# Kernel optimization log

Measured on AMD Instinct MI355X. Metric: run time of the kernel, lower is better.

## Reference

```python
import jax, jax.numpy as jnp
import numpy as np

SIM_THRESHOLD = 0.9


def setup_inputs() -> dict:
    key = jax.random.key(0)
    k1, k2 = jax.random.split(key)
    # patches: b * c * num * ws * ws  (b=2, c=8, num=1024, ws=3) -> n = 16384
    patches = jax.random.normal(k1, (2, 8, 1024, 3, 3), dtype=jnp.float32)
    # db: m * ws * ws
    db = jax.random.normal(k2, (16384, 3, 3), dtype=jnp.float32)
    return {"patches": patches, "db": db}


def reference(patches, db):
    ws = patches.shape[-1]
    p = patches.reshape(-1, ws, ws)          # [n, ws, ws]
    n = p.shape[0]
    m = db.shape[0]
    pf = p.reshape(n, -1)                    # [n, ws*ws]
    df = db.reshape(m, -1)                   # [m, ws*ws]
    dot = pf @ df.T                          # [n, m], tiny K=ws*ws -> memory bound
    norm_n = jnp.linalg.norm(pf, axis=1, keepdims=True)   # [n, 1]
    norm_m = jnp.linalg.norm(df, axis=1, keepdims=True)   # [m, 1]
    cos = dot / (norm_n * norm_m.T)          # [n, m] cosine similarity
    # patch kept only if dissimilar to EVERY db entry
    mask = jnp.all(cos < SIM_THRESHOLD, axis=1)            # [n] bool
    # jit-friendly fixed-shape compaction: zero out rejected patches instead of
    # dropping rows (original does db = cat(db, patches[mask]))
    filtered = jnp.where(mask[:, None, None], p, jnp.zeros((), p.dtype))
    return jnp.concatenate([db.reshape(-1, ws, ws), filtered], axis=0)  # [m+n, ws, ws]
```

## Files before the change

### kernel.cpp

```cpp
#include <hip/hip_runtime.h>

#define NPATCH 16384
#define NDB    16384
#define WS9    9
#define KP     16
#define JCH    32
#define CHUNK  (NDB / JCH)
#define TILES  (CHUNK / 32)
#define BAND_LO 0.89998f
#define BAND_HI 0.90002f
#define COPY_BLOCKS 144

typedef short bf16x8 __attribute__((ext_vector_type(8)));
typedef float f32x16 __attribute__((ext_vector_type(16)));

__device__ __forceinline__ float np_norm9(const float* v) {
#pragma clang fp contract(off)
    float q0 = v[0] * v[0], q1 = v[1] * v[1], q2 = v[2] * v[2], q3 = v[3] * v[3];
    float q4 = v[4] * v[4], q5 = v[5] * v[5], q6 = v[6] * v[6], q7 = v[7] * v[7];
    float q8 = v[8] * v[8];
    float s = ((q0 + q1) + (q2 + q3)) + ((q4 + q5) + (q6 + q7));
    s = s + q8;
    return sqrtf(s);
}

__device__ __forceinline__ unsigned short f2bf(float x) {
    unsigned u = __float_as_uint(x);
    return (unsigned short)((u + 0x7fffu + ((u >> 16) & 1u)) >> 16);
}
__device__ __forceinline__ float bf2f(unsigned short h) {
    return __uint_as_float(((unsigned)h) << 16);
}

__device__ __forceinline__ void stage_row(const float* __restrict__ src,
                                          unsigned short* dh, unsigned short* dl) {
    float v[WS9];
#pragma unroll
    for (int k = 0; k < WS9; k++) v[k] = src[k];
    float inv = 1.0f / np_norm9(v);
    unsigned short h[KP], l[KP];
#pragma unroll
    for (int k = 0; k < KP; k++) {
        float x = (k < WS9) ? v[k] * inv : 0.0f;
        h[k] = f2bf(x);
        l[k] = f2bf(x - bf2f(h[k]));
    }
    int hw[8], lw[8];
#pragma unroll
    for (int k = 0; k < 8; k++) {
        hw[k] = (int)h[2 * k] | ((int)h[2 * k + 1] << 16);
        lw[k] = (int)l[2 * k] | ((int)l[2 * k + 1] << 16);
    }
    ((int4*)dh)[0] = make_int4(hw[0], hw[1], hw[2], hw[3]);
    ((int4*)dh)[1] = make_int4(hw[4], hw[5], hw[6], hw[7]);
    ((int4*)dl)[0] = make_int4(lw[0], lw[1], lw[2], lw[3]);
    ((int4*)dl)[1] = make_int4(lw[4], lw[5], lw[6], lw[7]);
}

__global__ __launch_bounds__(256) void k_phase1(const float* __restrict__ patches,
                                                const float* __restrict__ db,
                                                float* __restrict__ partial,
                                                int* __restrict__ band_count) {
    __shared__ __align__(16) unsigned short s_dnh[CHUNK * KP];
    __shared__ __align__(16) unsigned short s_dnl[CHUNK * KP];
    __shared__ __align__(16) unsigned short s_pnh[256 * KP];
    __shared__ __align__(16) unsigned short s_pnl[256 * KP];

    if (blockIdx.x == 0 && blockIdx.y == 0 && threadIdx.x == 0) *band_count = 0;

    int jbase = blockIdx.y * CHUNK;
    int ibase = blockIdx.x * 256;
#pragma unroll
    for (int rr = 0; rr < CHUNK / 256; rr++) {
        int r = rr * 256 + threadIdx.x;
        stage_row(db + (size_t)(jbase + r) * WS9, &s_dnh[r * KP], &s_dnl[r * KP]);
    }
    stage_row(patches + (size_t)(ibase + threadIdx.x) * WS9,
              &s_pnh[threadIdx.x * KP], &s_pnl[threadIdx.x * KP]);
    __syncthreads();

    int lane = threadIdx.x & 63;
    int wave = threadIdx.x >> 6;
    int col = lane & 31;
    int half = lane >> 5;
    int i0 = ibase + wave * 64;

    const bf16x8* Ph = (const bf16x8*)s_pnh;
    const bf16x8* Pl = (const bf16x8*)s_pnl;
    bf16x8 b_hi0 = Ph[(wave * 64 + col) * 2 + half];
    bf16x8 b_lo0 = Pl[(wave * 64 + col) * 2 + half];
    bf16x8 b_hi1 = Ph[(wave * 64 + 32 + col) * 2 + half];
    bf16x8 b_lo1 = Pl[(wave * 64 + 32 + col) * 2 + half];

    const bf16x8* Ah = (const bf16x8*)s_dnh;
    const bf16x8* Al = (const bf16x8*)s_dnl;

    f32x16 zc = {0.f,0.f,0.f,0.f,0.f,0.f,0.f,0.f,0.f,0.f,0.f,0.f,0.f,0.f,0.f,0.f};
    float rm0 = -3.0e38f, rm1 = -3.0e38f;

#pragma unroll 2
    for (int t = 0; t < TILES; ++t) {
        bf16x8 a_h = Ah[(t * 32 + col) * 2 + half];
        bf16x8 a_l = Al[(t * 32 + col) * 2 + half];
        f32x16 acc0 = __builtin_amdgcn_mfma_f32_32x32x16_bf16(a_h, b_hi0, zc, 0, 0, 0);
        acc0 = __builtin_amdgcn_mfma_f32_32x32x16_bf16(a_h, b_lo0, acc0, 0, 0, 0);
        acc0 = __builtin_amdgcn_mfma_f32_32x32x16_bf16(a_l, b_hi0, acc0, 0, 0, 0);
        f32x16 acc1 = __builtin_amdgcn_mfma_f32_32x32x16_bf16(a_h, b_hi1, zc, 0, 0, 0);
        acc1 = __builtin_amdgcn_mfma_f32_32x32x16_bf16(a_h, b_lo1, acc1, 0, 0, 0);
        acc1 = __builtin_amdgcn_mfma_f32_32x32x16_bf16(a_l, b_hi1, acc1, 0, 0, 0);
#pragma unroll
        for (int r = 0; r < 16; ++r) {
            rm0 = fmaxf(rm0, acc0[r]);
            rm1 = fmaxf(rm1, acc1[r]);
        }
    }
    rm0 = fmaxf(rm0, __shfl_xor(rm0, 32, 64));
    rm1 = fmaxf(rm1, __shfl_xor(rm1, 32, 64));
    int ti = half ? (i0 + 32 + col) : (i0 + col);
    partial[(size_t)blockIdx.y * NPATCH + ti] = half ? rm1 : rm0;
}

__global__ __launch_bounds__(256) void k_finish(const float* __restrict__ patches,
                                                const float* __restrict__ db,
                                                const float* __restrict__ partial,
                                                float* __restrict__ out,
                                                int* __restrict__ band_list,
                                                int* __restrict__ band_count) {
    int b = blockIdx.x;
    if (b < COPY_BLOCKS) {
        int e = b * 256 + threadIdx.x;
        ((float4*)out)[e] = ((const float4*)db)[e];
        return;
    }
    int i = (b - COPY_BLOCKS) * 256 + threadIdx.x;
    float cosmax = partial[i];
#pragma unroll
    for (int c = 1; c < JCH; c++)
        cosmax = fmaxf(cosmax, partial[(size_t)c * NPATCH + i]);
    if (cosmax >= BAND_LO && cosmax < BAND_HI) {
        int idx = atomicAdd(band_count, 1);
        band_list[idx] = i;
        return;
    }
    int hit = (cosmax >= BAND_HI) ? 1 : 0;
#pragma unroll
    for (int k = 0; k < WS9; k++)
        out[(size_t)(NDB + i) * WS9 + k] = hit ? 0.0f : patches[(size_t)i * WS9 + k];
}

__global__ __launch_bounds__(256) void k_phase2(const float* __restrict__ patches,
                                                const float* __restrict__ db,
                                                const int* __restrict__ band_list,
                                                const int* __restrict__ band_count,
                                                float* __restrict__ out) {
    __shared__ float sp[WS9];
    __shared__ float snp;
    __shared__ int shit;
    int nb = *band_count;
    for (int idx = blockIdx.x; idx < nb; idx += gridDim.x) {
        int i = band_list[idx];
        if (threadIdx.x == 0) {
            float p[WS9];
            for (int k = 0; k < WS9; k++) { p[k] = patches[(size_t)i * WS9 + k]; sp[k] = p[k]; }
            snp = np_norm9(p);
            shit = 0;
        }
        __syncthreads();
        float p[WS9];
#pragma unroll
        for (int k = 0; k < WS9; k++) p[k] = sp[k];
        float npn = snp;
        int hit = 0;
        for (int j = (int)threadIdx.x; j < NDB; j += 256) {
            float d[WS9];
#pragma unroll
            for (int k = 0; k < WS9; k++) d[k] = db[(size_t)j * WS9 + k];
            float dot = 0.0f;
#pragma unroll
            for (int k = 0; k < WS9; k++) dot = fmaf(p[k], d[k], dot);
            float nd = np_norm9(d);
            float cs = dot / (npn * nd);
            if (!((double)cs < 0.9)) hit = 1;
        }
        if (hit) atomicOr(&shit, 1);
        __syncthreads();
        int m = shit;
        if (threadIdx.x < WS9)
            out[(size_t)(NDB + i) * WS9 + threadIdx.x] = m ? 0.0f : sp[threadIdx.x];
        __syncthreads();
    }
}

extern "C" void kernel_launch(void* const* d_in, const int* in_sizes, int n_in,
                              void* d_out, int out_size, void* d_ws, size_t ws_size,
                              hipStream_t stream) {
    const float* patches = (const float*)d_in[0];
    const float* db      = (const float*)d_in[1];
    float* out = (float*)d_out;

    char* wsb = (char*)d_ws;
    float* partial    = (float*)wsb;
    int*   band_list  = (int*)(wsb + (size_t)JCH * NPATCH * 4);
    int*   band_count = (int*)(wsb + (size_t)JCH * NPATCH * 4 + (size_t)NPATCH * 4);

    k_phase1<<<dim3(NPATCH / 256, JCH), dim3(256), 0, stream>>>(patches, db,
                                                                partial, band_count);
    k_finish<<<dim3(COPY_BLOCKS + NPATCH / 256), dim3(256), 0, stream>>>(
        patches, db, partial, out, band_list, band_count);
    k_phase2<<<dim3(256), dim3(256), 0, stream>>>(patches, db, band_list, band_count, out);
}
```

Before: 95.38 us.

## Precompute normalized bf16 hi/lo splits once in a prep kernel

Adds a prep kernel that normalizes and splits all patches and db rows into bf16 hi/lo pairs once, and also copies db into the output. Previously every phase1 block recomputed norms and splits for its db chunk and patches. Phase1 now loads the pre-split data from global memory with int4 copies into shared memory and reads the patch operands directly from global. The running max reduction is rewritten as a tree of 3-input max ops. The cost is an extra kernel launch plus workspace traffic for the staged arrays.

```diff
diff --git a/kernel.cpp b/kernel.cpp
--- a/kernel.cpp
+++ b/kernel.cpp
@@ -9,10 +9,12 @@
 #define TILES  (CHUNK / 32)
 #define BAND_LO 0.89998f
 #define BAND_HI 0.90002f
-#define COPY_BLOCKS 144
+#define PREP_BLOCKS 144
 
 typedef short bf16x8 __attribute__((ext_vector_type(8)));
 typedef float f32x16 __attribute__((ext_vector_type(16)));
+
+#define MAX3(a,b,c) fmaxf(fmaxf((a),(b)),(c))
 
 __device__ __forceinline__ float np_norm9(const float* v) {
 #pragma clang fp contract(off)
@@ -57,27 +59,48 @@
     ((int4*)dl)[1] = make_int4(lw[4], lw[5], lw[6], lw[7]);
 }
 
-__global__ __launch_bounds__(256) void k_phase1(const float* __restrict__ patches,
-                                                const float* __restrict__ db,
-                                                float* __restrict__ partial,
-                                                int* __restrict__ band_count) {
-    __shared__ __align__(16) unsigned short s_dnh[CHUNK * KP];
-    __shared__ __align__(16) unsigned short s_dnl[CHUNK * KP];
-    __shared__ __align__(16) unsigned short s_pnh[256 * KP];
-    __shared__ __align__(16) unsigned short s_pnl[256 * KP];
-
-    if (blockIdx.x == 0 && blockIdx.y == 0 && threadIdx.x == 0) *band_count = 0;
+__global__ __launch_bounds__(256) void k_prep(const float* __restrict__ patches,
+                                              const float* __restrict__ db,
+                                              unsigned short* __restrict__ pnh,
+                                              unsigned short* __restrict__ pnl,
+                                              unsigned short* __restrict__ dnh,
+                                              unsigned short* __restrict__ dnl,
+                                              float* __restrict__ out,
+                                              int* __restrict__ band_count) {
+    int t = blockIdx.x * 256 + threadIdx.x;
+    if (t == 0) *band_count = 0;
+    ((float4*)out)[t] = ((const float4*)db)[t];
+    if (t < NPATCH) {
+        stage_row(patches + (size_t)t * WS9, &pnh[(size_t)t * KP], &pnl[(size_t)t * KP]);
+    } else if (t < 2 * NPATCH) {
+        int r = t - NPATCH;
+        stage_row(db + (size_t)r * WS9, &dnh[(size_t)r * KP], &dnl[(size_t)r * KP]);
+    }
+}
+
+__global__ __launch_bounds__(256) void k_phase1(const unsigned short* __restrict__ pnh,
+                                                const unsigned short* __restrict__ pnl,
+                                                const unsigned short* __restrict__ dnh,
+                                                const unsigned short* __restrict__ dnl,
+                                                float* __restrict__ partial) {
+    __shared__ __align__(16) unsigned short s_dh[CHUNK * KP];
+    __shared__ __align__(16) unsigned short s_dl[CHUNK * KP];
 
     int jbase = blockIdx.y * CHUNK;
     int ibase = blockIdx.x * 256;
-#pragma unroll
-    for (int rr = 0; rr < CHUNK / 256; rr++) {
-        int r = rr * 256 + threadIdx.x;
-        stage_row(db + (size_t)(jbase + r) * WS9, &s_dnh[r * KP], &s_dnl[r * KP]);
-    }
-    stage_row(patches + (size_t)(ibase + threadIdx.x) * WS9,
-              &s_pnh[threadIdx.x * KP], &s_pnl[threadIdx.x * KP]);
-    __syncthreads();
+
+    {
+        const int4* gh = (const int4*)(dnh + (size_t)jbase * KP);
+        const int4* gl = (const int4*)(dnl + (size_t)jbase * KP);
+        int4* sh = (int4*)s_dh;
+        int4* sl = (int4*)s_dl;
+#pragma unroll
+        for (int u = 0; u < 4; u++) {
+            int e = u * 256 + threadIdx.x;
+            sh[e] = gh[e];
+            sl[e] = gl[e];
+        }
+    }
 
     int lane = threadIdx.x & 63;
     int wave = threadIdx.x >> 6;
@@ -85,15 +108,17 @@
     int half = lane >> 5;
     int i0 = ibase + wave * 64;
 
-    const bf16x8* Ph = (const bf16x8*)s_pnh;
-    const bf16x8* Pl = (const bf16x8*)s_pnl;
-    bf16x8 b_hi0 = Ph[(wave * 64 + col) * 2 + half];
-    bf16x8 b_lo0 = Pl[(wave * 64 + col) * 2 + half];
-    bf16x8 b_hi1 = Ph[(wave * 64 + 32 + col) * 2 + half];
-    bf16x8 b_lo1 = Pl[(wave * 64 + 32 + col) * 2 + half];
-
-    const bf16x8* Ah = (const bf16x8*)s_dnh;
-    const bf16x8* Al = (const bf16x8*)s_dnl;
+    const bf16x8* Ph = (const bf16x8*)pnh;
+    const bf16x8* Pl = (const bf16x8*)pnl;
+    bf16x8 b_hi0 = Ph[(size_t)(i0 + col) * 2 + half];
+    bf16x8 b_lo0 = Pl[(size_t)(i0 + col) * 2 + half];
+    bf16x8 b_hi1 = Ph[(size_t)(i0 + 32 + col) * 2 + half];
+    bf16x8 b_lo1 = Pl[(size_t)(i0 + 32 + col) * 2 + half];
+
+    __syncthreads();
+
+    const bf16x8* Ah = (const bf16x8*)s_dh;
+    const bf16x8* Al = (const bf16x8*)s_dl;
 
     f32x16 zc = {0.f,0.f,0.f,0.f,0.f,0.f,0.f,0.f,0.f,0.f,0.f,0.f,0.f,0.f,0.f,0.f};
     float rm0 = -3.0e38f, rm1 = -3.0e38f;
@@ -108,10 +133,25 @@
         f32x16 acc1 = __builtin_amdgcn_mfma_f32_32x32x16_bf16(a_h, b_hi1, zc, 0, 0, 0);
         acc1 = __builtin_amdgcn_mfma_f32_32x32x16_bf16(a_h, b_lo1, acc1, 0, 0, 0);
         acc1 = __builtin_amdgcn_mfma_f32_32x32x16_bf16(a_l, b_hi1, acc1, 0, 0, 0);
-#pragma unroll
-        for (int r = 0; r < 16; ++r) {
-            rm0 = fmaxf(rm0, acc0[r]);
-            rm1 = fmaxf(rm1, acc1[r]);
+        {
+            float u0 = MAX3(acc0[0],  acc0[1],  acc0[2]);
+            float u1 = MAX3(acc0[3],  acc0[4],  acc0[5]);
+            float u2 = MAX3(acc0[6],  acc0[7],  acc0[8]);
+            float u3 = MAX3(acc0[9],  acc0[10], acc0[11]);
+            float u4 = MAX3(acc0[12], acc0[13], acc0[14]);
+            float u5 = MAX3(u0, u1, acc0[15]);
+            float u6 = MAX3(u2, u3, u4);
+            rm0 = MAX3(u5, u6, rm0);
+        }
+        {
+            float u0 = MAX3(acc1[0],  acc1[1],  acc1[2]);
+            float u1 = MAX3(acc1[3],  acc1[4],  acc1[5]);
+            float u2 = MAX3(acc1[6],  acc1[7],  acc1[8]);
+            float u3 = MAX3(acc1[9],  acc1[10], acc1[11]);
+            float u4 = MAX3(acc1[12], acc1[13], acc1[14]);
+            float u5 = MAX3(u0, u1, acc1[15]);
+            float u6 = MAX3(u2, u3, u4);
+            rm1 = MAX3(u5, u6, rm1);
         }
     }
     rm0 = fmaxf(rm0, __shfl_xor(rm0, 32, 64));
@@ -120,19 +160,12 @@
     partial[(size_t)blockIdx.y * NPATCH + ti] = half ? rm1 : rm0;
 }
 
-__global__ __launch_bounds__(256) void k_finish(const float* __restrict__ patches,
-                                                const float* __restrict__ db,
-                                                const float* __restrict__ partial,
-                                                float* __restrict__ out,
-                                                int* __restrict__ band_list,
-                                                int* __restrict__ band_count) {
-    int b = blockIdx.x;
-    if (b < COPY_BLOCKS) {
-        int e = b * 256 + threadIdx.x;
-        ((float4*)out)[e] = ((const float4*)db)[e];
-        return;
-    }
-    int i = (b - COPY_BLOCKS) * 256 + threadIdx.x;
+__global__ __launch_bounds__(256) void k_classify(const float* __restrict__ patches,
+                                                  const float* __restrict__ partial,
+                                                  float* __restrict__ out,
+                                                  int* __restrict__ band_list,
+                                                  int* __restrict__ band_count) {
+    int i = blockIdx.x * 256 + threadIdx.x;
     float cosmax = partial[i];
 #pragma unroll
     for (int c = 1; c < JCH; c++)
@@ -199,13 +232,27 @@
     float* out = (float*)d_out;
 
     char* wsb = (char*)d_ws;
-    float* partial    = (float*)wsb;
-    int*   band_list  = (int*)(wsb + (size_t)JCH * NPATCH * 4);
-    int*   band_count = (int*)(wsb + (size_t)JCH * NPATCH * 4 + (size_t)NPATCH * 4);
-
-    k_phase1<<<dim3(NPATCH / 256, JCH), dim3(256), 0, stream>>>(patches, db,
-                                                                partial, band_count);
-    k_finish<<<dim3(COPY_BLOCKS + NPATCH / 256), dim3(256), 0, stream>>>(
-        patches, db, partial, out, band_list, band_count);
+    size_t o_partial = 0;
+    size_t o_blist   = (size_t)JCH * NPATCH * 4;
+    size_t o_bcount  = o_blist + (size_t)NPATCH * 4;
+    size_t o_pnh     = o_bcount + 256;
+    size_t o_pnl     = o_pnh + (size_t)NPATCH * KP * 2;
+    size_t o_dnh     = o_pnl + (size_t)NPATCH * KP * 2;
+    size_t o_dnl     = o_dnh + (size_t)NDB * KP * 2;
+
+    float* partial          = (float*)(wsb + o_partial);
+    int*   band_list        = (int*)(wsb + o_blist);
+    int*   band_count       = (int*)(wsb + o_bcount);
+    unsigned short* pnh     = (unsigned short*)(wsb + o_pnh);
+    unsigned short* pnl     = (unsigned short*)(wsb + o_pnl);
+    unsigned short* dnh     = (unsigned short*)(wsb + o_dnh);
+    unsigned short* dnl     = (unsigned short*)(wsb + o_dnl);
+
+    k_prep<<<dim3(PREP_BLOCKS), dim3(256), 0, stream>>>(patches, db, pnh, pnl,
+                                                        dnh, dnl, out, band_count);
+    k_phase1<<<dim3(NPATCH / 256, JCH), dim3(256), 0, stream>>>(pnh, pnl, dnh, dnl,
+                                                                partial);
+    k_classify<<<dim3(NPATCH / 256), dim3(256), 0, stream>>>(patches, partial, out,
+                                                             band_list, band_count);
     k_phase2<<<dim3(256), dim3(256), 0, stream>>>(patches, db, band_list, band_count, out);
 }
```

Result: slower. 101.5 us (+6.4%).

## Widen patch tile per block, reuse LDS, and fold band recheck into finish kernel

Applied to the files above, without the earlier changes.

Each phase-1 block now handles 512 patches, with each wave computing four 32x32 MFMA output tiles per db tile instead of two. Patch fragments are held in registers so the same LDS buffer can then hold the db chunk. This halves the grid along the patch axis and reuses each staged db tile across more patches, and the per-tile max reduction now uses max3 chains. The separate band-recheck kernel is removed: ambiguous patches are listed in shared memory and rechecked exactly inside k_finish, using db norms that phase 1 writes out. That saves a launch, the global atomics and the recomputed norms, but serialises any band patches within one finish block.

```diff
diff --git a/kernel.cpp b/kernel.cpp
--- a/kernel.cpp
+++ b/kernel.cpp
@@ -5,14 +5,17 @@
 #define WS9    9
 #define KP     16
 #define JCH    32
-#define CHUNK  (NDB / JCH)
+#define CHUNK  512
 #define TILES  (CHUNK / 32)
+#define PBLK   512
 #define BAND_LO 0.89998f
 #define BAND_HI 0.90002f
 #define COPY_BLOCKS 144
 
 typedef short bf16x8 __attribute__((ext_vector_type(8)));
 typedef float f32x16 __attribute__((ext_vector_type(16)));
+
+#define MAX3(a,b,c) fmaxf(fmaxf((a),(b)),(c))
 
 __device__ __forceinline__ float np_norm9(const float* v) {
 #pragma clang fp contract(off)
@@ -33,11 +36,14 @@
 }
 
 __device__ __forceinline__ void stage_row(const float* __restrict__ src,
-                                          unsigned short* dh, unsigned short* dl) {
+                                          unsigned short* dh, unsigned short* dl,
+                                          float* nrm_out) {
     float v[WS9];
 #pragma unroll
     for (int k = 0; k < WS9; k++) v[k] = src[k];
-    float inv = 1.0f / np_norm9(v);
+    float nrm = np_norm9(v);
+    float inv = 1.0f / nrm;
+    *nrm_out = nrm;
     unsigned short h[KP], l[KP];
 #pragma unroll
     for (int k = 0; k < KP; k++) {
@@ -60,108 +66,145 @@
 __global__ __launch_bounds__(256) void k_phase1(const float* __restrict__ patches,
                                                 const float* __restrict__ db,
                                                 float* __restrict__ partial,
-                                                int* __restrict__ band_count) {
-    __shared__ __align__(16) unsigned short s_dnh[CHUNK * KP];
-    __shared__ __align__(16) unsigned short s_dnl[CHUNK * KP];
-    __shared__ __align__(16) unsigned short s_pnh[256 * KP];
-    __shared__ __align__(16) unsigned short s_pnl[256 * KP];
-
-    if (blockIdx.x == 0 && blockIdx.y == 0 && threadIdx.x == 0) *band_count = 0;
+                                                float* __restrict__ dbnorm) {
+    __shared__ __align__(16) unsigned short s_h[CHUNK * KP];
+    __shared__ __align__(16) unsigned short s_l[CHUNK * KP];
 
     int jbase = blockIdx.y * CHUNK;
-    int ibase = blockIdx.x * 256;
-#pragma unroll
-    for (int rr = 0; rr < CHUNK / 256; rr++) {
-        int r = rr * 256 + threadIdx.x;
-        stage_row(db + (size_t)(jbase + r) * WS9, &s_dnh[r * KP], &s_dnl[r * KP]);
-    }
-    stage_row(patches + (size_t)(ibase + threadIdx.x) * WS9,
-              &s_pnh[threadIdx.x * KP], &s_pnl[threadIdx.x * KP]);
-    __syncthreads();
-
-    int lane = threadIdx.x & 63;
-    int wave = threadIdx.x >> 6;
+    int ibase = blockIdx.x * PBLK;
+    int tid = (int)threadIdx.x;
+
+#pragma unroll
+    for (int rr = 0; rr < PBLK / 256; rr++) {
+        int r = rr * 256 + tid;
+        float nrm;
+        stage_row(patches + (size_t)(ibase + r) * WS9, &s_h[r * KP], &s_l[r * KP], &nrm);
+    }
+    __syncthreads();
+
+    int lane = tid & 63;
+    int wave = tid >> 6;
     int col = lane & 31;
     int half = lane >> 5;
-    int i0 = ibase + wave * 64;
-
-    const bf16x8* Ph = (const bf16x8*)s_pnh;
-    const bf16x8* Pl = (const bf16x8*)s_pnl;
-    bf16x8 b_hi0 = Ph[(wave * 64 + col) * 2 + half];
-    bf16x8 b_lo0 = Pl[(wave * 64 + col) * 2 + half];
-    bf16x8 b_hi1 = Ph[(wave * 64 + 32 + col) * 2 + half];
-    bf16x8 b_lo1 = Pl[(wave * 64 + 32 + col) * 2 + half];
-
-    const bf16x8* Ah = (const bf16x8*)s_dnh;
-    const bf16x8* Al = (const bf16x8*)s_dnl;
+    int i0 = ibase + wave * 128;
+
+    const bf16x8* Ph = (const bf16x8*)s_h;
+    const bf16x8* Pl = (const bf16x8*)s_l;
+    bf16x8 bh0 = Ph[(wave * 128 +  0 + col) * 2 + half];
+    bf16x8 bh1 = Ph[(wave * 128 + 32 + col) * 2 + half];
+    bf16x8 bh2 = Ph[(wave * 128 + 64 + col) * 2 + half];
+    bf16x8 bh3 = Ph[(wave * 128 + 96 + col) * 2 + half];
+    bf16x8 bl0 = Pl[(wave * 128 +  0 + col) * 2 + half];
+    bf16x8 bl1 = Pl[(wave * 128 + 32 + col) * 2 + half];
+    bf16x8 bl2 = Pl[(wave * 128 + 64 + col) * 2 + half];
+    bf16x8 bl3 = Pl[(wave * 128 + 96 + col) * 2 + half];
+    __syncthreads();
+
+#pragma unroll
+    for (int rr = 0; rr < CHUNK / 256; rr++) {
+        int r = rr * 256 + tid;
+        float nrm;
+        stage_row(db + (size_t)(jbase + r) * WS9, &s_h[r * KP], &s_l[r * KP], &nrm);
+        if (blockIdx.x == 0) dbnorm[jbase + r] = nrm;
+    }
+    __syncthreads();
+
+    const bf16x8* Ah = (const bf16x8*)s_h;
+    const bf16x8* Al = (const bf16x8*)s_l;
 
     f32x16 zc = {0.f,0.f,0.f,0.f,0.f,0.f,0.f,0.f,0.f,0.f,0.f,0.f,0.f,0.f,0.f,0.f};
-    float rm0 = -3.0e38f, rm1 = -3.0e38f;
-
-#pragma unroll 2
+    float rm0 = -3.0e38f, rm1 = -3.0e38f, rm2 = -3.0e38f, rm3 = -3.0e38f;
+
+#define REDUCE(acc, rm)                                                     \
+    {                                                                       \
+        float u0 = MAX3(acc[0],  acc[1],  acc[2]);                          \
+        float u1 = MAX3(acc[3],  acc[4],  acc[5]);                          \
+        float u2 = MAX3(acc[6],  acc[7],  acc[8]);                          \
+        float u3 = MAX3(acc[9],  acc[10], acc[11]);                         \
+        float u4 = MAX3(acc[12], acc[13], acc[14]);                         \
+        float u5 = MAX3(u0, u1, acc[15]);                                   \
+        float u6 = MAX3(u2, u3, u4);                                        \
+        rm = MAX3(u5, u6, rm);                                              \
+    }
+
     for (int t = 0; t < TILES; ++t) {
         bf16x8 a_h = Ah[(t * 32 + col) * 2 + half];
         bf16x8 a_l = Al[(t * 32 + col) * 2 + half];
-        f32x16 acc0 = __builtin_amdgcn_mfma_f32_32x32x16_bf16(a_h, b_hi0, zc, 0, 0, 0);
-        acc0 = __builtin_amdgcn_mfma_f32_32x32x16_bf16(a_h, b_lo0, acc0, 0, 0, 0);
-        acc0 = __builtin_amdgcn_mfma_f32_32x32x16_bf16(a_l, b_hi0, acc0, 0, 0, 0);
-        f32x16 acc1 = __builtin_amdgcn_mfma_f32_32x32x16_bf16(a_h, b_hi1, zc, 0, 0, 0);
-        acc1 = __builtin_amdgcn_mfma_f32_32x32x16_bf16(a_h, b_lo1, acc1, 0, 0, 0);
-        acc1 = __builtin_amdgcn_mfma_f32_32x32x16_bf16(a_l, b_hi1, acc1, 0, 0, 0);
-#pragma unroll
-        for (int r = 0; r < 16; ++r) {
-            rm0 = fmaxf(rm0, acc0[r]);
-            rm1 = fmaxf(rm1, acc1[r]);
-        }
-    }
+        f32x16 acc0 = __builtin_amdgcn_mfma_f32_32x32x16_bf16(a_h, bh0, zc, 0, 0, 0);
+        f32x16 acc1 = __builtin_amdgcn_mfma_f32_32x32x16_bf16(a_h, bh1, zc, 0, 0, 0);
+        f32x16 acc2 = __builtin_amdgcn_mfma_f32_32x32x16_bf16(a_h, bh2, zc, 0, 0, 0);
+        f32x16 acc3 = __builtin_amdgcn_mfma_f32_32x32x16_bf16(a_h, bh3, zc, 0, 0, 0);
+        acc0 = __builtin_amdgcn_mfma_f32_32x32x16_bf16(a_h, bl0, acc0, 0, 0, 0);
+        acc1 = __builtin_amdgcn_mfma_f32_32x32x16_bf16(a_h, bl1, acc1, 0, 0, 0);
+        acc2 = __builtin_amdgcn_mfma_f32_32x32x16_bf16(a_h, bl2, acc2, 0, 0, 0);
+        acc3 = __builtin_amdgcn_mfma_f32_32x32x16_bf16(a_h, bl3, acc3, 0, 0, 0);
+        acc0 = __builtin_amdgcn_mfma_f32_32x32x16_bf16(a_l, bh0, acc0, 0, 0, 0);
+        acc1 = __builtin_amdgcn_mfma_f32_32x32x16_bf16(a_l, bh1, acc1, 0, 0, 0);
+        acc2 = __builtin_amdgcn_mfma_f32_32x32x16_bf16(a_l, bh2, acc2, 0, 0, 0);
+        acc3 = __builtin_amdgcn_mfma_f32_32x32x16_bf16(a_l, bh3, acc3, 0, 0, 0);
+        REDUCE(acc0, rm0)
+        REDUCE(acc1, rm1)
+        REDUCE(acc2, rm2)
+        REDUCE(acc3, rm3)
+    }
+#undef REDUCE
+
     rm0 = fmaxf(rm0, __shfl_xor(rm0, 32, 64));
     rm1 = fmaxf(rm1, __shfl_xor(rm1, 32, 64));
-    int ti = half ? (i0 + 32 + col) : (i0 + col);
-    partial[(size_t)blockIdx.y * NPATCH + ti] = half ? rm1 : rm0;
+    rm2 = fmaxf(rm2, __shfl_xor(rm2, 32, 64));
+    rm3 = fmaxf(rm3, __shfl_xor(rm3, 32, 64));
+    float w0 = half ? rm2 : rm0;
+    float w1 = half ? rm3 : rm1;
+    int t0 = half ? (i0 + 64 + col) : (i0 + col);
+    int t1 = half ? (i0 + 96 + col) : (i0 + 32 + col);
+    size_t prow = (size_t)blockIdx.y * NPATCH;
+    partial[prow + t0] = w0;
+    partial[prow + t1] = w1;
 }
 
 __global__ __launch_bounds__(256) void k_finish(const float* __restrict__ patches,
                                                 const float* __restrict__ db,
                                                 const float* __restrict__ partial,
-                                                float* __restrict__ out,
-                                                int* __restrict__ band_list,
-                                                int* __restrict__ band_count) {
+                                                const float* __restrict__ dbnorm,
+                                                float* __restrict__ out) {
     int b = blockIdx.x;
     if (b < COPY_BLOCKS) {
         int e = b * 256 + threadIdx.x;
         ((float4*)out)[e] = ((const float4*)db)[e];
         return;
     }
-    int i = (b - COPY_BLOCKS) * 256 + threadIdx.x;
+    __shared__ int s_bn;
+    __shared__ int s_blist[256];
+    __shared__ float sp[WS9];
+    __shared__ float snp;
+    __shared__ int shit;
+
+    int tid = (int)threadIdx.x;
+    int i = (b - COPY_BLOCKS) * 256 + tid;
+    if (tid == 0) s_bn = 0;
+    __syncthreads();
+
     float cosmax = partial[i];
 #pragma unroll
     for (int c = 1; c < JCH; c++)
         cosmax = fmaxf(cosmax, partial[(size_t)c * NPATCH + i]);
     if (cosmax >= BAND_LO && cosmax < BAND_HI) {
-        int idx = atomicAdd(band_count, 1);
-        band_list[idx] = i;
-        return;
-    }
-    int hit = (cosmax >= BAND_HI) ? 1 : 0;
-#pragma unroll
-    for (int k = 0; k < WS9; k++)
-        out[(size_t)(NDB + i) * WS9 + k] = hit ? 0.0f : patches[(size_t)i * WS9 + k];
-}
-
-__global__ __launch_bounds__(256) void k_phase2(const float* __restrict__ patches,
-                                                const float* __restrict__ db,
-                                                const int* __restrict__ band_list,
-                                                const int* __restrict__ band_count,
-                                                float* __restrict__ out) {
-    __shared__ float sp[WS9];
-    __shared__ float snp;
-    __shared__ int shit;
-    int nb = *band_count;
-    for (int idx = blockIdx.x; idx < nb; idx += gridDim.x) {
-        int i = band_list[idx];
-        if (threadIdx.x == 0) {
+        int idx = atomicAdd(&s_bn, 1);
+        s_blist[idx] = i;
+    } else {
+        int hit = (cosmax >= BAND_HI) ? 1 : 0;
+#pragma unroll
+        for (int k = 0; k < WS9; k++)
+            out[(size_t)(NDB + i) * WS9 + k] = hit ? 0.0f : patches[(size_t)i * WS9 + k];
+    }
+    __syncthreads();
+    int nb = s_bn;
+
+    for (int e = 0; e < nb; e++) {
+        int bi = s_blist[e];
+        if (tid == 0) {
             float p[WS9];
-            for (int k = 0; k < WS9; k++) { p[k] = patches[(size_t)i * WS9 + k]; sp[k] = p[k]; }
+            for (int k = 0; k < WS9; k++) { p[k] = patches[(size_t)bi * WS9 + k]; sp[k] = p[k]; }
             snp = np_norm9(p);
             shit = 0;
         }
@@ -171,22 +214,21 @@
         for (int k = 0; k < WS9; k++) p[k] = sp[k];
         float npn = snp;
         int hit = 0;
-        for (int j = (int)threadIdx.x; j < NDB; j += 256) {
+        for (int j = tid; j < NDB; j += 256) {
             float d[WS9];
 #pragma unroll
             for (int k = 0; k < WS9; k++) d[k] = db[(size_t)j * WS9 + k];
             float dot = 0.0f;
 #pragma unroll
             for (int k = 0; k < WS9; k++) dot = fmaf(p[k], d[k], dot);
-            float nd = np_norm9(d);
-            float cs = dot / (npn * nd);
+            float cs = dot / (npn * dbnorm[j]);
             if (!((double)cs < 0.9)) hit = 1;
         }
         if (hit) atomicOr(&shit, 1);
         __syncthreads();
         int m = shit;
-        if (threadIdx.x < WS9)
-            out[(size_t)(NDB + i) * WS9 + threadIdx.x] = m ? 0.0f : sp[threadIdx.x];
+        if (tid < WS9)
+            out[(size_t)(NDB + bi) * WS9 + tid] = m ? 0.0f : sp[tid];
         __syncthreads();
     }
 }
@@ -199,13 +241,11 @@
     float* out = (float*)d_out;
 
     char* wsb = (char*)d_ws;
-    float* partial    = (float*)wsb;
-    int*   band_list  = (int*)(wsb + (size_t)JCH * NPATCH * 4);
-    int*   band_count = (int*)(wsb + (size_t)JCH * NPATCH * 4 + (size_t)NPATCH * 4);
-
-    k_phase1<<<dim3(NPATCH / 256, JCH), dim3(256), 0, stream>>>(patches, db,
-                                                                partial, band_count);
+    float* partial = (float*)wsb;
+    float* dbnorm  = (float*)(wsb + (size_t)JCH * NPATCH * 4);
+
+    k_phase1<<<dim3(NPATCH / PBLK, JCH), dim3(256), 0, stream>>>(patches, db,
+                                                                 partial, dbnorm);
     k_finish<<<dim3(COPY_BLOCKS + NPATCH / 256), dim3(256), 0, stream>>>(
-        patches, db, partial, out, band_list, band_count);
-    k_phase2<<<dim3(256), dim3(256), 0, stream>>>(patches, db, band_list, band_count, out);
-}
+        patches, db, partial, dbnorm, out);
+}
```

Result: no change. 96.64 us (+1.3%).

## Fuse band-recheck pass into finish kernel and use 3-input max reduction

Applied to the files above, without the earlier changes.

Removes the separate phase-2 kernel launch by having each finish block keep a shared-memory list of its near-threshold patches and recheck them exactly in place. This drops one kernel launch and the global atomic counter and list. It also rewrites the per-tile max reduction as a tree of 3-input fmax calls so the compiler can emit v_max3 instructions. The catch is that any block holding band patches now serially scans the whole db, and only 64 blocks do this work, where the old pass spread it over 256 blocks.

```diff
diff --git a/kernel.cpp b/kernel.cpp
--- a/kernel.cpp
+++ b/kernel.cpp
@@ -14,6 +14,8 @@
 typedef short bf16x8 __attribute__((ext_vector_type(8)));
 typedef float f32x16 __attribute__((ext_vector_type(16)));
 
+#define MAX3(a,b,c) fmaxf(fmaxf((a),(b)),(c))
+
 __device__ __forceinline__ float np_norm9(const float* v) {
 #pragma clang fp contract(off)
     float q0 = v[0] * v[0], q1 = v[1] * v[1], q2 = v[2] * v[2], q3 = v[3] * v[3];
@@ -59,14 +61,11 @@
 
 __global__ __launch_bounds__(256) void k_phase1(const float* __restrict__ patches,
                                                 const float* __restrict__ db,
-                                                float* __restrict__ partial,
-                                                int* __restrict__ band_count) {
+                                                float* __restrict__ partial) {
     __shared__ __align__(16) unsigned short s_dnh[CHUNK * KP];
     __shared__ __align__(16) unsigned short s_dnl[CHUNK * KP];
     __shared__ __align__(16) unsigned short s_pnh[256 * KP];
     __shared__ __align__(16) unsigned short s_pnl[256 * KP];
-
-    if (blockIdx.x == 0 && blockIdx.y == 0 && threadIdx.x == 0) *band_count = 0;
 
     int jbase = blockIdx.y * CHUNK;
     int ibase = blockIdx.x * 256;
@@ -108,10 +107,25 @@
         f32x16 acc1 = __builtin_amdgcn_mfma_f32_32x32x16_bf16(a_h, b_hi1, zc, 0, 0, 0);
         acc1 = __builtin_amdgcn_mfma_f32_32x32x16_bf16(a_h, b_lo1, acc1, 0, 0, 0);
         acc1 = __builtin_amdgcn_mfma_f32_32x32x16_bf16(a_l, b_hi1, acc1, 0, 0, 0);
-#pragma unroll
-        for (int r = 0; r < 16; ++r) {
-            rm0 = fmaxf(rm0, acc0[r]);
-            rm1 = fmaxf(rm1, acc1[r]);
+        {
+            float u0 = MAX3(acc0[0],  acc0[1],  acc0[2]);
+            float u1 = MAX3(acc0[3],  acc0[4],  acc0[5]);
+            float u2 = MAX3(acc0[6],  acc0[7],  acc0[8]);
+            float u3 = MAX3(acc0[9],  acc0[10], acc0[11]);
+            float u4 = MAX3(acc0[12], acc0[13], acc0[14]);
+            float u5 = MAX3(u0, u1, acc0[15]);
+            float u6 = MAX3(u2, u3, u4);
+            rm0 = MAX3(u5, u6, rm0);
+        }
+        {
+            float u0 = MAX3(acc1[0],  acc1[1],  acc1[2]);
+            float u1 = MAX3(acc1[3],  acc1[4],  acc1[5]);
+            float u2 = MAX3(acc1[6],  acc1[7],  acc1[8]);
+            float u3 = MAX3(acc1[9],  acc1[10], acc1[11]);
+            float u4 = MAX3(acc1[12], acc1[13], acc1[14]);
+            float u5 = MAX3(u0, u1, acc1[15]);
+            float u6 = MAX3(u2, u3, u4);
+            rm1 = MAX3(u5, u6, rm1);
         }
     }
     rm0 = fmaxf(rm0, __shfl_xor(rm0, 32, 64));
@@ -123,45 +137,45 @@
 __global__ __launch_bounds__(256) void k_finish(const float* __restrict__ patches,
                                                 const float* __restrict__ db,
                                                 const float* __restrict__ partial,
-                                                float* __restrict__ out,
-                                                int* __restrict__ band_list,
-                                                int* __restrict__ band_count) {
+                                                float* __restrict__ out) {
     int b = blockIdx.x;
     if (b < COPY_BLOCKS) {
         int e = b * 256 + threadIdx.x;
         ((float4*)out)[e] = ((const float4*)db)[e];
         return;
     }
-    int i = (b - COPY_BLOCKS) * 256 + threadIdx.x;
+    __shared__ int s_bn;
+    __shared__ int s_blist[256];
+    __shared__ float sp[WS9];
+    __shared__ float snp;
+    __shared__ int shit;
+
+    int tid = (int)threadIdx.x;
+    int i = (b - COPY_BLOCKS) * 256 + tid;
+    if (tid == 0) s_bn = 0;
+    __syncthreads();
+
     float cosmax = partial[i];
 #pragma unroll
     for (int c = 1; c < JCH; c++)
         cosmax = fmaxf(cosmax, partial[(size_t)c * NPATCH + i]);
     if (cosmax >= BAND_LO && cosmax < BAND_HI) {
-        int idx = atomicAdd(band_count, 1);
-        band_list[idx] = i;
-        return;
-    }
-    int hit = (cosmax >= BAND_HI) ? 1 : 0;
-#pragma unroll
-    for (int k = 0; k < WS9; k++)
-        out[(size_t)(NDB + i) * WS9 + k] = hit ? 0.0f : patches[(size_t)i * WS9 + k];
-}
-
-__global__ __launch_bounds__(256) void k_phase2(const float* __restrict__ patches,
-                                                const float* __restrict__ db,
-                                                const int* __restrict__ band_list,
-                                                const int* __restrict__ band_count,
-                                                float* __restrict__ out) {
-    __shared__ float sp[WS9];
-    __shared__ float snp;
-    __shared__ int shit;
-    int nb = *band_count;
-    for (int idx = blockIdx.x; idx < nb; idx += gridDim.x) {
-        int i = band_list[idx];
-        if (threadIdx.x == 0) {
+        int idx = atomicAdd(&s_bn, 1);
+        s_blist[idx] = i;
+    } else {
+        int hit = (cosmax >= BAND_HI) ? 1 : 0;
+#pragma unroll
+        for (int k = 0; k < WS9; k++)
+            out[(size_t)(NDB + i) * WS9 + k] = hit ? 0.0f : patches[(size_t)i * WS9 + k];
+    }
+    __syncthreads();
+    int nb = s_bn;
+
+    for (int e = 0; e < nb; e++) {
+        int bi = s_blist[e];
+        if (tid == 0) {
             float p[WS9];
-            for (int k = 0; k < WS9; k++) { p[k] = patches[(size_t)i * WS9 + k]; sp[k] = p[k]; }
+            for (int k = 0; k < WS9; k++) { p[k] = patches[(size_t)bi * WS9 + k]; sp[k] = p[k]; }
             snp = np_norm9(p);
             shit = 0;
         }
@@ -171,7 +185,7 @@
         for (int k = 0; k < WS9; k++) p[k] = sp[k];
         float npn = snp;
         int hit = 0;
-        for (int j = (int)threadIdx.x; j < NDB; j += 256) {
+        for (int j = tid; j < NDB; j += 256) {
             float d[WS9];
 #pragma unroll
             for (int k = 0; k < WS9; k++) d[k] = db[(size_t)j * WS9 + k];
@@ -185,8 +199,8 @@
         if (hit) atomicOr(&shit, 1);
         __syncthreads();
         int m = shit;
-        if (threadIdx.x < WS9)
-            out[(size_t)(NDB + i) * WS9 + threadIdx.x] = m ? 0.0f : sp[threadIdx.x];
+        if (tid < WS9)
+            out[(size_t)(NDB + bi) * WS9 + tid] = m ? 0.0f : sp[tid];
         __syncthreads();
     }
 }
@@ -198,14 +212,9 @@
     const float* db      = (const float*)d_in[1];
     float* out = (float*)d_out;
 
-    char* wsb = (char*)d_ws;
-    float* partial    = (float*)wsb;
-    int*   band_list  = (int*)(wsb + (size_t)JCH * NPATCH * 4);
-    int*   band_count = (int*)(wsb + (size_t)JCH * NPATCH * 4 + (size_t)NPATCH * 4);
-
-    k_phase1<<<dim3(NPATCH / 256, JCH), dim3(256), 0, stream>>>(patches, db,
-                                                                partial, band_count);
+    float* partial = (float*)d_ws;
+
+    k_phase1<<<dim3(NPATCH / 256, JCH), dim3(256), 0, stream>>>(patches, db, partial);
     k_finish<<<dim3(COPY_BLOCKS + NPATCH / 256), dim3(256), 0, stream>>>(
-        patches, db, partial, out, band_list, band_count);
-    k_phase2<<<dim3(256), dim3(256), 0, stream>>>(patches, db, band_list, band_count, out);
-}
+        patches, db, partial, out);
+}
```

New measurement: 94.41 us. About the same (-1.0%).
